# Kernel optimization log

Measured on AMD Instinct MI355X. Metric: run time of the kernel, lower is better.

Reference implementation:

```python
import jax, jax.numpy as jnp
import numpy as np

# ---- static configuration (matches init_kwargs) ----
D_MODEL = 512
N_HEAD = 16
HEAD_DIM = D_MODEL // N_HEAD
SCALE = HEAD_DIM ** -0.5
SIZE = (64, 64)
WINDOW = (8, 8)
SHIFT = (4, 4)
WS = WINDOW[0] * WINDOW[1]          # tokens per window = 64
NW = (SIZE[0] // WINDOW[0]) * (SIZE[1] // WINDOW[1])  # windows per sample = 64


def _rel_pos_index(window):
    w0, w1 = window
    coords = np.stack(np.meshgrid(np.arange(w0), np.arange(w1), indexing='ij')).reshape(2, -1)
    rel = (coords[:, :, None] - coords[:, None, :]).transpose(1, 2, 0)  # [ws, ws, 2]
    rel[:, :, 0] += w0 - 1
    rel[:, :, 1] += w1 - 1
    rel[:, :, 0] *= 2 * w1 - 1
    return rel.sum(-1)  # [ws, ws] in [0, (2w0-1)(2w1-1))


def _shift_mask(size, window, shift):
    # Swin-style attention mask for shifted windows: 1.0 where tokens belong
    # to different cyclic-shift regions, else 0.0. Shape [nw, ws, ws].
    H, W = size
    w0, w1 = window
    s0, s1 = shift
    img = np.zeros((H, W))
    cnt = 0
    h_slices = (slice(0, -w0), slice(-w0, -s0), slice(-s0, None)) if s0 > 0 else (slice(None),)
    w_slices = (slice(0, -w1), slice(-w1, -s1), slice(-s1, None)) if s1 > 0 else (slice(None),)
    for hs in h_slices:
        for ws_ in w_slices:
            img[hs, ws_] = cnt
            cnt += 1
    win = img.reshape(H // w0, w0, W // w1, w1).transpose(0, 2, 1, 3).reshape(-1, w0 * w1)
    return (win[:, None, :] != win[:, :, None]).astype(np.float32)


REL_IDX = jnp.asarray(_rel_pos_index(WINDOW))              # [ws, ws] int
MASK = jnp.asarray(-100.0 * _shift_mask(SIZE, WINDOW, SHIFT))  # [nw, ws, ws]


def setup_inputs() -> dict:
    key = jax.random.key(0)
    k1, k2, k3, k4 = jax.random.split(key, 4)
    x = jax.random.normal(k1, (8, SIZE[0], SIZE[1], D_MODEL), dtype=jnp.float32)
    qkv_w = jax.random.normal(k2, (3 * D_MODEL, D_MODEL), dtype=jnp.float32) * (D_MODEL ** -0.5)
    qkv_b = jax.random.normal(k3, (3 * D_MODEL,), dtype=jnp.float32) * 0.02
    bias_table = jax.random.normal(k4, ((2 * WINDOW[0] - 1) * (2 * WINDOW[1] - 1), N_HEAD), dtype=jnp.float32) * 0.02
    return {"x": x, "qkv_w": qkv_w, "qkv_b": qkv_b, "bias_table": bias_table}


def reference(x, qkv_w, qkv_b, bias_table):
    n, H, W, c = x.shape
    w0, w1 = WINDOW
    # --- window partition: [n, H, W, c] -> [n*nw, ws, c] ---
    part = x.reshape(n, H // w0, w0, W // w1, w1, c)
    part = part.transpose(0, 1, 3, 2, 4, 5).reshape(n * NW, WS, c)
    # --- qkv projection ---
    qkv = (part @ qkv_w.T + qkv_b).reshape(n * NW, WS, 3, N_HEAD, HEAD_DIM)
    q, k, v = qkv[:, :, 0] * SCALE, qkv[:, :, 1], qkv[:, :, 2]
    # --- scores + relative bias + shift mask + softmax ---
    attn = jnp.einsum('wihd,wjhd->whij', q, k)  # [n*nw, nh, ws, ws]
    bias = bias_table[REL_IDX].transpose(2, 0, 1)  # [nh, ws, ws]
    attn = attn.reshape(n, NW, N_HEAD, WS, WS) + bias[None, None] + MASK[None, :, None]
    attn = jax.nn.softmax(attn, axis=-1).reshape(n * NW, N_HEAD, WS, WS)
    # --- AV + unpartition ---
    out = jnp.einsum('whij,wjhd->wihd', attn, v).reshape(n * NW, WS, c)
    out = out.reshape(n, H // w0, W // w1, w0, w1, c)
    return out.transpose(0, 1, 3, 2, 4, 5).reshape(n, H, W, c)
```

## Files before the change

kernel.cpp:

```cpp
#include <hip/hip_runtime.h>
#include <stdint.h>

typedef unsigned short u16;
typedef __attribute__((ext_vector_type(4))) float floatx4;
typedef __attribute__((ext_vector_type(8))) short bf16x8;

#define MTOK   32768
#define KDIM   512
#define NQKV   1536
#define NWIN   512
#define N_HEAD 16
#define QK_SCALE 0.17677669529663687f

__device__ __forceinline__ u16 f2bf(float f) {
  union { float f; unsigned u; } v; v.f = f;
  unsigned r = v.u + 0x7fffu + ((v.u >> 16) & 1u);
  return (u16)(r >> 16);
}

__device__ __forceinline__ void load_lds16(const void* g, void* l) {
  __builtin_amdgcn_global_load_lds((const __attribute__((address_space(1))) void*)g,
                                   (__attribute__((address_space(3))) void*)l,
                                   16, 0, 0);
}

__global__ __launch_bounds__(256) void convert_x(const float* __restrict__ x,
                                                 u16* __restrict__ A) {
  int idx = blockIdx.x * 256 + threadIdx.x;
  int e = idx * 4;
  int c = e & 511;
  int tg = e >> 9;
  int w = tg >> 6, t = tg & 63;
  int img = w >> 6, wy = (w >> 3) & 7, wx = w & 7;
  int ty = t >> 3, tx = t & 7;
  int y = wy * 8 + ty, xp = wx * 8 + tx;
  const float4 v = *(const float4*)(x + (((img * 64 + y) * 64 + xp) * 512 + c));
  ushort4 o;
  o.x = f2bf(v.x); o.y = f2bf(v.y); o.z = f2bf(v.z); o.w = f2bf(v.w);
  *(ushort4*)(A + e) = o;
}

__global__ __launch_bounds__(256) void convert_w(const float* __restrict__ wsrc,
                                                 u16* __restrict__ Wb) {
  int e = (blockIdx.x * 256 + threadIdx.x) * 4;
  const float4 v = *(const float4*)(wsrc + e);
  ushort4 o;
  o.x = f2bf(v.x); o.y = f2bf(v.y); o.z = f2bf(v.z); o.w = f2bf(v.w);
  *(ushort4*)(Wb + e) = o;
}

__global__ __launch_bounds__(256) void gemm_qkv(const u16* __restrict__ A,
                                                const u16* __restrict__ Wb,
                                                const float* __restrict__ bias,
                                                u16* __restrict__ QKV) {
  __shared__ __attribute__((aligned(16))) u16 lA[128 * 32];
  __shared__ __attribute__((aligned(16))) u16 lB[128 * 32];

  int b = blockIdx.x;
  int xcd = b & 7, slot = b >> 3;
  int mtile = (slot / 12) * 8 + xcd;
  int ntile = slot % 12;

  int tid = threadIdx.x;
  int wv = tid >> 6, lane = tid & 63;
  int il = lane & 15, ch = lane >> 4;
  int wm = (wv & 1) * 64, wn = (wv >> 1) * 64;

  floatx4 acc[4][4];
  floatx4 zacc = {0.f, 0.f, 0.f, 0.f};
#pragma unroll
  for (int m = 0; m < 4; ++m)
#pragma unroll
    for (int n = 0; n < 4; ++n) acc[m][n] = zacc;

  int row0 = tid >> 2, ch4 = tid & 3;
  const u16* Abase = A + (mtile * 128 + row0) * KDIM + ch4 * 8;
  const u16* Bbase = Wb + (ntile * 128 + row0) * KDIM + ch4 * 8;
  char* lAb = (char*)lA;
  char* lBb = (char*)lB;
  char* lA0 = lAb + wv * 1024;
  char* lA1 = lAb + 4096 + wv * 1024;
  char* lB0 = lBb + wv * 1024;
  char* lB1 = lBb + 4096 + wv * 1024;

  for (int kb = 0; kb < KDIM; kb += 32) {
    __syncthreads();
    load_lds16(Abase + kb, lA0);
    load_lds16(Abase + kb + 64 * KDIM, lA1);
    load_lds16(Bbase + kb, lB0);
    load_lds16(Bbase + kb + 64 * KDIM, lB1);
    __syncthreads();

    bf16x8 af[4], bfr[4];
#pragma unroll
    for (int mt = 0; mt < 4; ++mt)
      af[mt] = *(const bf16x8*)(lAb + (wm + mt * 16 + il) * 64 + ch * 16);
#pragma unroll
    for (int nt = 0; nt < 4; ++nt)
      bfr[nt] = *(const bf16x8*)(lBb + (wn + nt * 16 + il) * 64 + ch * 16);
#pragma unroll
    for (int mt = 0; mt < 4; ++mt)
#pragma unroll
      for (int nt = 0; nt < 4; ++nt)
        acc[mt][nt] = __builtin_amdgcn_mfma_f32_16x16x32_bf16(af[mt], bfr[nt], acc[mt][nt], 0, 0, 0);
  }

#pragma unroll
  for (int nt = 0; nt < 4; ++nt) {
    int col = ntile * 128 + wn + nt * 16 + il;
    float bv = bias[col];
#pragma unroll
    for (int mt = 0; mt < 4; ++mt) {
      int rbase = mtile * 128 + wm + mt * 16 + ch * 4;
#pragma unroll
      for (int r = 0; r < 4; ++r)
        QKV[(rbase + r) * NQKV + col] = f2bf(acc[mt][nt][r] + bv);
    }
  }
}

__global__ __launch_bounds__(256) void attn(const u16* __restrict__ QKV,
                                            const float* __restrict__ btab,
                                            float* __restrict__ out) {
  __shared__ __attribute__((aligned(16))) u16 Pl[64 * 88];
  __shared__ __attribute__((aligned(16))) u16 Vt[32 * 88];
  __shared__ float sbias[225];

  int bid = blockIdx.x;
  int w = bid >> 4, h = bid & 15;
  int tid = threadIdx.x;

  {
    int j = tid >> 2, dbase = (tid & 3) * 8;
    const u16* vp = QKV + (w * 64 + j) * NQKV + 1024 + h * 32 + dbase;
    union { uint4 v; u16 s[8]; } u;
    u.v = *(const uint4*)vp;
#pragma unroll
    for (int q = 0; q < 8; ++q) Vt[(dbase + q) * 88 + j] = u.s[q];
  }
  if (tid < 225) sbias[tid] = btab[tid * 16 + h];

  int lane = tid & 63, wv = tid >> 6;
  int il = lane & 15, ch = lane >> 4;
  const u16* qkw = QKV + (w * 64) * NQKV;

  bf16x8 aq = *(const bf16x8*)(qkw + (wv * 16 + il) * NQKV + h * 32 + ch * 8);
  floatx4 zacc = {0.f, 0.f, 0.f, 0.f};
  floatx4 s[4];
#pragma unroll
  for (int jt = 0; jt < 4; ++jt) {
    bf16x8 bk = *(const bf16x8*)(qkw + (jt * 16 + il) * NQKV + 512 + h * 32 + ch * 8);
    s[jt] = __builtin_amdgcn_mfma_f32_16x16x32_bf16(aq, bk, zacc, 0, 0, 0);
  }

  __syncthreads();

  int winidx = w & 63;
  int wy = winidx >> 3, wx = winidx & 7;
  float val[4][4];
#pragma unroll
  for (int r = 0; r < 4; ++r) {
    int i = wv * 16 + ch * 4 + r;
    int ty = i >> 3, tx = i & 7;
    int ry = (wy == 7) ? (ty < 4 ? 1 : 2) : 0;
    int rx = (wx == 7) ? (tx < 4 ? 1 : 2) : 0;
    int li = ry * 3 + rx;
#pragma unroll
    for (int jt = 0; jt < 4; ++jt) {
      int j = jt * 16 + il;
      int sy = j >> 3, sx = j & 7;
      int rjy = (wy == 7) ? (sy < 4 ? 1 : 2) : 0;
      int rjx = (wx == 7) ? (sx < 4 ? 1 : 2) : 0;
      float v = s[jt][r] * QK_SCALE + sbias[(ty - sy + 7) * 15 + (tx - sx + 7)];
      if (li != (rjy * 3 + rjx)) v -= 100.0f;
      val[r][jt] = v;
    }
  }

#pragma unroll
  for (int r = 0; r < 4; ++r) {
    float m = fmaxf(fmaxf(val[r][0], val[r][1]), fmaxf(val[r][2], val[r][3]));
    m = fmaxf(m, __shfl_xor(m, 1, 64));
    m = fmaxf(m, __shfl_xor(m, 2, 64));
    m = fmaxf(m, __shfl_xor(m, 4, 64));
    m = fmaxf(m, __shfl_xor(m, 8, 64));
    float sum = 0.f;
#pragma unroll
    for (int jt = 0; jt < 4; ++jt) { val[r][jt] = __expf(val[r][jt] - m); sum += val[r][jt]; }
    sum += __shfl_xor(sum, 1, 64);
    sum += __shfl_xor(sum, 2, 64);
    sum += __shfl_xor(sum, 4, 64);
    sum += __shfl_xor(sum, 8, 64);
    float inv = 1.0f / sum;
    int i = wv * 16 + ch * 4 + r;
#pragma unroll
    for (int jt = 0; jt < 4; ++jt)
      Pl[i * 88 + jt * 16 + il] = f2bf(val[r][jt] * inv);
  }

  __syncthreads();

  floatx4 o0 = zacc, o1 = zacc;
#pragma unroll
  for (int kk = 0; kk < 2; ++kk) {
    bf16x8 ap  = *(const bf16x8*)((const u16*)Pl + (wv * 16 + il) * 88 + kk * 32 + ch * 8);
    bf16x8 bv0 = *(const bf16x8*)((const u16*)Vt + il * 88 + kk * 32 + ch * 8);
    bf16x8 bv1 = *(const bf16x8*)((const u16*)Vt + (16 + il) * 88 + kk * 32 + ch * 8);
    o0 = __builtin_amdgcn_mfma_f32_16x16x32_bf16(ap, bv0, o0, 0, 0, 0);
    o1 = __builtin_amdgcn_mfma_f32_16x16x32_bf16(ap, bv1, o1, 0, 0, 0);
  }

  int img = w >> 6;
#pragma unroll
  for (int r = 0; r < 4; ++r) {
    int i = wv * 16 + ch * 4 + r;
    int ty = i >> 3, tx = i & 7;
    int y = wy * 8 + ty, xp = wx * 8 + tx;
    float* op = out + ((img * 64 + y) * 64 + xp) * 512 + h * 32;
    op[il] = o0[r];
    op[16 + il] = o1[r];
  }
}

extern "C" void kernel_launch(void* const* d_in, const int* in_sizes, int n_in,
                              void* d_out, int out_size, void* d_ws, size_t ws_size,
                              hipStream_t stream) {
  const float* x      = (const float*)d_in[0];
  const float* qkv_w  = (const float*)d_in[1];
  const float* qkv_b  = (const float*)d_in[2];
  const float* btab   = (const float*)d_in[3];
  float* out = (float*)d_out;

  char* ws = (char*)d_ws;
  u16* A   = (u16*)ws;
  u16* Wb  = (u16*)(ws + (size_t)MTOK * KDIM * 2);
  u16* QKV = (u16*)(ws + (size_t)MTOK * KDIM * 2 + (size_t)NQKV * KDIM * 2);

  convert_x<<<dim3(MTOK * KDIM / 1024), dim3(256), 0, stream>>>(x, A);
  convert_w<<<dim3(NQKV * KDIM / 1024), dim3(256), 0, stream>>>(qkv_w, Wb);
  gemm_qkv<<<dim3(3072), dim3(256), 0, stream>>>(A, Wb, qkv_b, QKV);
  attn<<<dim3(NWIN * N_HEAD), dim3(256), 0, stream>>>(QKV, btab, out);
}
```

Measured before the change: 241.9 us.

## Write QKV in per-window-head layout with pre-transposed V and swizzled LDS

The GEMM epilogue stages the output tile through LDS and writes Q, K and V into separate contiguous per-(window, head) sections. Q is pre-scaled by the attention scale and V is stored transposed, so the attention kernel reads contiguous 4KB blocks instead of strided rows and no longer transposes V in LDS. The GEMM LDS loads also use an XOR swizzle to reduce bank conflicts. This costs an extra LDS round trip and sync in the GEMM epilogue.

```diff
diff --git a/kernel.cpp b/kernel.cpp
--- a/kernel.cpp
+++ b/kernel.cpp
@@ -10,6 +10,7 @@
 #define NQKV   1536
 #define NWIN   512
 #define N_HEAD 16
+#define SECSZ  (512 * 16 * 2048)
 #define QK_SCALE 0.17677669529663687f
 
 __device__ __forceinline__ u16 f2bf(float f) {
@@ -53,8 +54,8 @@
                                                 const u16* __restrict__ Wb,
                                                 const float* __restrict__ bias,
                                                 u16* __restrict__ QKV) {
-  __shared__ __attribute__((aligned(16))) u16 lA[128 * 32];
-  __shared__ __attribute__((aligned(16))) u16 lB[128 * 32];
+  __shared__ __attribute__((aligned(16))) char smem[34816];
+  u16* Ct = (u16*)smem;
 
   int b = blockIdx.x;
   int xcd = b & 7, slot = b >> 3;
@@ -73,16 +74,18 @@
 #pragma unroll
     for (int n = 0; n < 4; ++n) acc[m][n] = zacc;
 
-  int row0 = tid >> 2, ch4 = tid & 3;
+  int row0 = tid >> 2;
+  int ch4 = (tid & 3) ^ (row0 & 3);
   const u16* Abase = A + (mtile * 128 + row0) * KDIM + ch4 * 8;
   const u16* Bbase = Wb + (ntile * 128 + row0) * KDIM + ch4 * 8;
-  char* lAb = (char*)lA;
-  char* lBb = (char*)lB;
+  char* lAb = smem;
+  char* lBb = smem + 8192;
   char* lA0 = lAb + wv * 1024;
   char* lA1 = lAb + 4096 + wv * 1024;
   char* lB0 = lBb + wv * 1024;
   char* lB1 = lBb + 4096 + wv * 1024;
 
+  int sw = il & 3;
   for (int kb = 0; kb < KDIM; kb += 32) {
     __syncthreads();
     load_lds16(Abase + kb, lA0);
@@ -94,10 +97,10 @@
     bf16x8 af[4], bfr[4];
 #pragma unroll
     for (int mt = 0; mt < 4; ++mt)
-      af[mt] = *(const bf16x8*)(lAb + (wm + mt * 16 + il) * 64 + ch * 16);
+      af[mt] = *(const bf16x8*)(lAb + (wm + mt * 16 + il) * 64 + (ch ^ sw) * 16);
 #pragma unroll
     for (int nt = 0; nt < 4; ++nt)
-      bfr[nt] = *(const bf16x8*)(lBb + (wn + nt * 16 + il) * 64 + ch * 16);
+      bfr[nt] = *(const bf16x8*)(lBb + (wn + nt * 16 + il) * 64 + (ch ^ sw) * 16);
 #pragma unroll
     for (int mt = 0; mt < 4; ++mt)
 #pragma unroll
@@ -105,16 +108,59 @@
         acc[mt][nt] = __builtin_amdgcn_mfma_f32_16x16x32_bf16(af[mt], bfr[nt], acc[mt][nt], 0, 0, 0);
   }
 
-#pragma unroll
-  for (int nt = 0; nt < 4; ++nt) {
-    int col = ntile * 128 + wn + nt * 16 + il;
-    float bv = bias[col];
-#pragma unroll
-    for (int mt = 0; mt < 4; ++mt) {
-      int rbase = mtile * 128 + wm + mt * 16 + ch * 4;
-#pragma unroll
-      for (int r = 0; r < 4; ++r)
-        QKV[(rbase + r) * NQKV + col] = f2bf(acc[mt][nt][r] + bv);
+  __syncthreads();
+
+  int sec = ntile >> 2;
+  int h0 = (ntile & 3) * 4;
+  int gw0 = mtile * 2;
+  u16* dst = QKV + (size_t)sec * SECSZ;
+
+  if (sec < 2) {
+    float sc = (sec == 0) ? QK_SCALE : 1.0f;
+#pragma unroll
+    for (int nt = 0; nt < 4; ++nt) {
+      float bv = bias[ntile * 128 + wn + nt * 16 + il];
+      int cl = wn + nt * 16 + il;
+#pragma unroll
+      for (int mt = 0; mt < 4; ++mt) {
+        int T0 = wm + mt * 16 + ch * 4;
+#pragma unroll
+        for (int r = 0; r < 4; ++r)
+          Ct[(T0 + r) * 136 + cl] = f2bf((acc[mt][nt][r] + bv) * sc);
+      }
+    }
+    __syncthreads();
+    int t_loc = tid >> 2, dc = tid & 3;
+#pragma unroll
+    for (int it = 0; it < 8; ++it) {
+      int wl = it >> 2, hl = it & 3;
+      uint4 v = *(const uint4*)(smem + (wl * 64 + t_loc) * 272 + hl * 64 + dc * 16);
+      *(uint4*)(dst + ((gw0 + wl) * 16 + h0 + hl) * 2048 + t_loc * 32 + dc * 8) = v;
+    }
+  } else {
+#pragma unroll
+    for (int nt = 0; nt < 4; ++nt) {
+      float bv = bias[ntile * 128 + wn + nt * 16 + il];
+      int cl = wn + nt * 16 + il;
+#pragma unroll
+      for (int mt = 0; mt < 4; ++mt) {
+        int T0 = wm + mt * 16 + ch * 4;
+        ushort4 p;
+        p.x = f2bf(acc[mt][nt][0] + bv);
+        p.y = f2bf(acc[mt][nt][1] + bv);
+        p.z = f2bf(acc[mt][nt][2] + bv);
+        p.w = f2bf(acc[mt][nt][3] + bv);
+        *(ushort4*)(Ct + cl * 136 + T0) = p;
+      }
+    }
+    __syncthreads();
+    int wl = tid >> 7, dd = (tid >> 3) & 15, tq = tid & 7;
+#pragma unroll
+    for (int it = 0; it < 8; ++it) {
+      int hl = it & 3, dh = it >> 2;
+      int d = dh * 16 + dd;
+      uint4 v = *(const uint4*)(smem + (hl * 32 + d) * 272 + wl * 128 + tq * 16);
+      *(uint4*)(dst + ((gw0 + wl) * 16 + h0 + hl) * 2048 + d * 64 + tq * 8) = v;
     }
   }
 }
@@ -123,33 +169,25 @@
                                             const float* __restrict__ btab,
                                             float* __restrict__ out) {
   __shared__ __attribute__((aligned(16))) u16 Pl[64 * 88];
-  __shared__ __attribute__((aligned(16))) u16 Vt[32 * 88];
   __shared__ float sbias[225];
 
   int bid = blockIdx.x;
   int w = bid >> 4, h = bid & 15;
   int tid = threadIdx.x;
-
-  {
-    int j = tid >> 2, dbase = (tid & 3) * 8;
-    const u16* vp = QKV + (w * 64 + j) * NQKV + 1024 + h * 32 + dbase;
-    union { uint4 v; u16 s[8]; } u;
-    u.v = *(const uint4*)vp;
-#pragma unroll
-    for (int q = 0; q < 8; ++q) Vt[(dbase + q) * 88 + j] = u.s[q];
-  }
   if (tid < 225) sbias[tid] = btab[tid * 16 + h];
 
   int lane = tid & 63, wv = tid >> 6;
   int il = lane & 15, ch = lane >> 4;
-  const u16* qkw = QKV + (w * 64) * NQKV;
-
-  bf16x8 aq = *(const bf16x8*)(qkw + (wv * 16 + il) * NQKV + h * 32 + ch * 8);
+  const u16* Qb = QKV + (w * 16 + h) * 2048;
+  const u16* Kb = Qb + SECSZ;
+  const u16* Vt = Qb + 2 * (size_t)SECSZ;
+
+  bf16x8 aq = *(const bf16x8*)(Qb + (wv * 16 + il) * 32 + ch * 8);
   floatx4 zacc = {0.f, 0.f, 0.f, 0.f};
   floatx4 s[4];
 #pragma unroll
   for (int jt = 0; jt < 4; ++jt) {
-    bf16x8 bk = *(const bf16x8*)(qkw + (jt * 16 + il) * NQKV + 512 + h * 32 + ch * 8);
+    bf16x8 bk = *(const bf16x8*)(Kb + (jt * 16 + il) * 32 + ch * 8);
     s[jt] = __builtin_amdgcn_mfma_f32_16x16x32_bf16(aq, bk, zacc, 0, 0, 0);
   }
 
@@ -171,7 +209,7 @@
       int sy = j >> 3, sx = j & 7;
       int rjy = (wy == 7) ? (sy < 4 ? 1 : 2) : 0;
       int rjx = (wx == 7) ? (sx < 4 ? 1 : 2) : 0;
-      float v = s[jt][r] * QK_SCALE + sbias[(ty - sy + 7) * 15 + (tx - sx + 7)];
+      float v = s[jt][r] + sbias[(ty - sy + 7) * 15 + (tx - sx + 7)];
       if (li != (rjy * 3 + rjx)) v -= 100.0f;
       val[r][jt] = v;
     }
@@ -204,8 +242,8 @@
 #pragma unroll
   for (int kk = 0; kk < 2; ++kk) {
     bf16x8 ap  = *(const bf16x8*)((const u16*)Pl + (wv * 16 + il) * 88 + kk * 32 + ch * 8);
-    bf16x8 bv0 = *(const bf16x8*)((const u16*)Vt + il * 88 + kk * 32 + ch * 8);
-    bf16x8 bv1 = *(const bf16x8*)((const u16*)Vt + (16 + il) * 88 + kk * 32 + ch * 8);
+    bf16x8 bv0 = *(const bf16x8*)(Vt + il * 64 + kk * 32 + ch * 8);
+    bf16x8 bv1 = *(const bf16x8*)(Vt + (16 + il) * 64 + kk * 32 + ch * 8);
     o0 = __builtin_amdgcn_mfma_f32_16x16x32_bf16(ap, bv0, o0, 0, 0, 0);
     o1 = __builtin_amdgcn_mfma_f32_16x16x32_bf16(ap, bv1, o1, 0, 0, 0);
   }
```

New measurement: 239.6 us. About the same (-0.9%).
